# Kernel tuning notes

Measured on AMD Instinct MI355X. Metric: run time of the kernel, lower is better.

## Reference

```python
import jax, jax.numpy as jnp
import numpy as np

N = 100000   # nodes
E = 600000   # edges
DIN = 128
H = 128
DOUT = 64
EPS = 1e-5   # BatchNorm1d default eps


def setup_inputs() -> dict:
    key = jax.random.key(0)
    ks = jax.random.split(key, 16)
    w = lambda k, shape: jax.random.normal(k, shape, jnp.float32) * 0.05
    return {
        "x": jax.random.normal(ks[0], (N, DIN), jnp.float32),
        "edge_index": jax.random.randint(ks[1], (2, E), 0, N),
        # layer 1: SAGEConv(DIN -> H)  (lin_l on aggregated neighbors w/ bias, lin_r on root)
        "Wl1": w(ks[2], (DIN, H)), "bl1": jnp.zeros((H,), jnp.float32), "Wr1": w(ks[3], (DIN, H)),
        "g1": jnp.ones((H,), jnp.float32), "be1": jnp.zeros((H,), jnp.float32),
        "rm1": jax.random.normal(ks[4], (H,), jnp.float32) * 0.1,
        "rv1": jax.random.uniform(ks[5], (H,), jnp.float32, 0.5, 1.5),
        # layer 2: SAGEConv(H -> H)
        "Wl2": w(ks[6], (H, H)), "bl2": jnp.zeros((H,), jnp.float32), "Wr2": w(ks[7], (H, H)),
        "g2": jnp.ones((H,), jnp.float32), "be2": jnp.zeros((H,), jnp.float32),
        "rm2": jax.random.normal(ks[8], (H,), jnp.float32) * 0.1,
        "rv2": jax.random.uniform(ks[9], (H,), jnp.float32, 0.5, 1.5),
        # layer 3: SAGEConv(H -> DOUT), no BN/ReLU after
        "Wl3": w(ks[10], (H, DOUT)), "bl3": jnp.zeros((DOUT,), jnp.float32), "Wr3": w(ks[11], (H, DOUT)),
    }


def _sage_conv(x, src, dst, Wl, bl, Wr):
    # mean-aggregate source features at targets, then lin_l(agg) + b + lin_r(x)
    agg = jax.ops.segment_sum(x[src], dst, num_segments=N)          # [N, d]
    deg = jax.ops.segment_sum(jnp.ones((src.shape[0],), x.dtype), dst, num_segments=N)
    agg = agg / jnp.maximum(deg, 1.0)[:, None]
    return agg @ Wl + bl + x @ Wr


def _bn_eval(h, g, b, rm, rv):
    return (h - rm) * (g * jax.lax.rsqrt(rv + EPS)) + b


def reference(x, edge_index, Wl1, bl1, Wr1, g1, be1, rm1, rv1,
              Wl2, bl2, Wr2, g2, be2, rm2, rv2, Wl3, bl3, Wr3):
    src, dst = edge_index[0], edge_index[1]
    h = jax.nn.relu(_bn_eval(_sage_conv(x, src, dst, Wl1, bl1, Wr1), g1, be1, rm1, rv1))
    h = jax.nn.relu(_bn_eval(_sage_conv(h, src, dst, Wl2, bl2, Wr2), g2, be2, rm2, rv2))
    return _sage_conv(h, src, dst, Wl3, bl3, Wr3)   # [N, DOUT]
```

## Files before the change

### kernel.cpp

```cpp
#include <hip/hip_runtime.h>

#define CAP 48

typedef short  s8v  __attribute__((ext_vector_type(8)));
typedef float  f4v  __attribute__((ext_vector_type(4)));

__device__ __forceinline__ unsigned short f2bf(float f) {
    unsigned u = __float_as_uint(f);
    u += 0x7FFFu + ((u >> 16) & 1u);
    return (unsigned short)(u >> 16);
}
__device__ __forceinline__ float bflo(unsigned v) { return __uint_as_float(v << 16); }
__device__ __forceinline__ float bfhi(unsigned v) { return __uint_as_float(v & 0xffff0000u); }

__global__ __launch_bounds__(256) void k_bucket(const int* __restrict__ src, const int* __restrict__ dst,
                                                int E, int* __restrict__ cnt, int* __restrict__ bucket) {
    int e = blockIdx.x * 256 + threadIdx.x;
    if (e < E) {
        int d = dst[e];
        int slot = atomicAdd(&cnt[d], 1);
        if (slot < CAP) bucket[(size_t)d * CAP + slot] = src[e];
    }
}

__global__ void k_prep(const float* g1, const float* be1, const float* rm1, const float* rv1, const float* bl1,
                       const float* g2, const float* be2, const float* rm2, const float* rv2, const float* bl2,
                       float* P) {
    int j = threadIdx.x;
    float s1 = g1[j] * rsqrtf(rv1[j] + 1e-5f);
    P[j]       = s1;
    P[128 + j] = (bl1[j] - rm1[j]) * s1 + be1[j];
    float s2 = g2[j] * rsqrtf(rv2[j] + 1e-5f);
    P[256 + j] = s2;
    P[384 + j] = (bl2[j] - rm2[j]) * s2 + be2[j];
}

__global__ __launch_bounds__(256) void k_cvt(const float* __restrict__ in, unsigned short* __restrict__ out, int n4) {
    int i = blockIdx.x * 256 + threadIdx.x;
    if (i < n4) {
        float4 v = ((const float4*)in)[i];
        ushort4 o;
        o.x = f2bf(v.x); o.y = f2bf(v.y); o.z = f2bf(v.z); o.w = f2bf(v.w);
        ((ushort4*)out)[i] = o;
    }
}

__global__ __launch_bounds__(256) void k_packW(const float* W0, const float* W1, const float* W2,
                                               const float* W3, const float* W4, const float* W5,
                                               unsigned short* P0, unsigned short* P1, unsigned short* P2,
                                               unsigned short* P3, unsigned short* P4, unsigned short* P5) {
    const float* W; unsigned short* P; int JD;
    switch (blockIdx.y) {
        case 0: W = W0; P = P0; JD = 128; break;
        case 1: W = W1; P = P1; JD = 128; break;
        case 2: W = W2; P = P2; JD = 128; break;
        case 3: W = W3; P = P3; JD = 128; break;
        case 4: W = W4; P = P4; JD = 64;  break;
        default:W = W5; P = P5; JD = 64;  break;
    }
    int o = blockIdx.x * 256 + threadIdx.x;
    if (o >= 128 * JD) return;
    int j    = o & 7;
    int lane = (o >> 3) & 63;
    int t    = o >> 9;
    int nt   = t % (JD / 16);
    int kt   = t / (JD / 16);
    int k = kt * 32 + (lane >> 4) * 8 + j;
    int n = nt * 16 + (lane & 15);
    P[o] = f2bf(W[(size_t)k * JD + n]);
}

__global__ __launch_bounds__(256) void k_agg128b(const unsigned short* __restrict__ in, const int* __restrict__ cnt,
                                                 const int* __restrict__ bucket, uint2* __restrict__ out, int n) {
    int wv   = (blockIdx.x * 256 + threadIdx.x) >> 6;
    int lane = threadIdx.x & 63;
    int g    = lane >> 5;
    int li   = lane & 31;
    int node = wv * 2 + g;
    if (node >= n) return;
    int c = cnt[node]; if (c > CAP) c = CAP;
    const uint2* inp = (const uint2*)in;
    int idxv = 0;
    if (li < c) idxv = bucket[(size_t)node * CAP + li];
    float a0 = 0.f, a1 = 0.f, a2 = 0.f, a3 = 0.f;
    const int base = g << 5;
    int cc = c < 32 ? c : 32;
    int s = 0;
    for (; s + 4 <= cc; s += 4) {
        int i0 = __shfl(idxv, base + s);
        int i1 = __shfl(idxv, base + s + 1);
        int i2 = __shfl(idxv, base + s + 2);
        int i3 = __shfl(idxv, base + s + 3);
        uint2 v0 = inp[(size_t)i0 * 32 + li];
        uint2 v1 = inp[(size_t)i1 * 32 + li];
        uint2 v2 = inp[(size_t)i2 * 32 + li];
        uint2 v3 = inp[(size_t)i3 * 32 + li];
        a0 += bflo(v0.x) + bflo(v1.x) + bflo(v2.x) + bflo(v3.x);
        a1 += bfhi(v0.x) + bfhi(v1.x) + bfhi(v2.x) + bfhi(v3.x);
        a2 += bflo(v0.y) + bflo(v1.y) + bflo(v2.y) + bflo(v3.y);
        a3 += bfhi(v0.y) + bfhi(v1.y) + bfhi(v2.y) + bfhi(v3.y);
    }
    for (; s < cc; s++) {
        int i0 = __shfl(idxv, base + s);
        uint2 v0 = inp[(size_t)i0 * 32 + li];
        a0 += bflo(v0.x); a1 += bfhi(v0.x); a2 += bflo(v0.y); a3 += bfhi(v0.y);
    }
    for (; s < c; s++) {
        int i0 = bucket[(size_t)node * CAP + s];
        uint2 v0 = inp[(size_t)i0 * 32 + li];
        a0 += bflo(v0.x); a1 += bfhi(v0.x); a2 += bflo(v0.y); a3 += bfhi(v0.y);
    }
    float iv = 1.0f / fmaxf((float)c, 1.0f);
    a0 *= iv; a1 *= iv; a2 *= iv; a3 *= iv;
    uint2 o;
    o.x = (unsigned)f2bf(a0) | ((unsigned)f2bf(a1) << 16);
    o.y = (unsigned)f2bf(a2) | ((unsigned)f2bf(a3) << 16);
    out[(size_t)node * 32 + li] = o;
}

__global__ __launch_bounds__(256) void k_agg64b(const unsigned short* __restrict__ in, const int* __restrict__ cnt,
                                                const int* __restrict__ bucket, float4* __restrict__ out, int n) {
    int wv   = (blockIdx.x * 256 + threadIdx.x) >> 6;
    int lane = threadIdx.x & 63;
    int g    = lane >> 4;
    int li   = lane & 15;
    int node = wv * 4 + g;
    if (node >= n) return;
    int c = cnt[node]; if (c > CAP) c = CAP;
    const uint2* inp = (const uint2*)in;
    int idxv = 0;
    if (li < c) idxv = bucket[(size_t)node * CAP + li];
    float a0 = 0.f, a1 = 0.f, a2 = 0.f, a3 = 0.f;
    const int base = g << 4;
    int cc = c < 16 ? c : 16;
    int s = 0;
    for (; s + 4 <= cc; s += 4) {
        int i0 = __shfl(idxv, base + s);
        int i1 = __shfl(idxv, base + s + 1);
        int i2 = __shfl(idxv, base + s + 2);
        int i3 = __shfl(idxv, base + s + 3);
        uint2 v0 = inp[(size_t)i0 * 16 + li];
        uint2 v1 = inp[(size_t)i1 * 16 + li];
        uint2 v2 = inp[(size_t)i2 * 16 + li];
        uint2 v3 = inp[(size_t)i3 * 16 + li];
        a0 += bflo(v0.x) + bflo(v1.x) + bflo(v2.x) + bflo(v3.x);
        a1 += bfhi(v0.x) + bfhi(v1.x) + bfhi(v2.x) + bfhi(v3.x);
        a2 += bflo(v0.y) + bflo(v1.y) + bflo(v2.y) + bflo(v3.y);
        a3 += bfhi(v0.y) + bfhi(v1.y) + bfhi(v2.y) + bfhi(v3.y);
    }
    for (; s < cc; s++) {
        int i0 = __shfl(idxv, base + s);
        uint2 v0 = inp[(size_t)i0 * 16 + li];
        a0 += bflo(v0.x); a1 += bfhi(v0.x); a2 += bflo(v0.y); a3 += bfhi(v0.y);
    }
    for (; s < c; s++) {
        int i0 = bucket[(size_t)node * CAP + s];
        uint2 v0 = inp[(size_t)i0 * 16 + li];
        a0 += bflo(v0.x); a1 += bfhi(v0.x); a2 += bflo(v0.y); a3 += bfhi(v0.y);
    }
    float iv = 1.0f / fmaxf((float)c, 1.0f);
    float4 o; o.x = a0 * iv; o.y = a1 * iv; o.z = a2 * iv; o.w = a3 * iv;
    out[(size_t)node * 16 + li] = o;
}

template<int JD, bool DUAL, bool RELU, bool ADDD, bool BIAS, bool OUTF, bool OUTB>
__global__ __launch_bounds__(256) void k_mfma(const unsigned short* __restrict__ A, const unsigned short* __restrict__ Bp,
                                              const unsigned short* __restrict__ A2, const unsigned short* __restrict__ B2p,
                                              const float* __restrict__ Dadd, const float* __restrict__ scale,
                                              const float* __restrict__ shift, float* __restrict__ outf,
                                              unsigned short* __restrict__ outb, int nrows) {
    constexpr int NT = JD / 16;
    constexpr int CW = JD / 32;
    constexpr int RG = 4 / CW;
    const int tid  = threadIdx.x;
    const int wave = tid >> 6;
    const int lane = tid & 63;
    const int cgrp = wave % CW;
    const int rgrp = wave / CW;
    const int rw0  = (blockIdx.x * RG + rgrp) * 32;
    if (rw0 >= nrows) return;

    const int m = lane & 15;
    const int q = lane >> 4;
    const int rA0 = min(rw0 + m,      nrows - 1);
    const int rA1 = min(rw0 + 16 + m, nrows - 1);
    const int nt0 = cgrp * 2;

    f4v acc[2][2];
    #pragma unroll
    for (int mt = 0; mt < 2; mt++)
        #pragma unroll
        for (int c = 0; c < 2; c++) {
            acc[mt][c][0] = 0.f; acc[mt][c][1] = 0.f; acc[mt][c][2] = 0.f; acc[mt][c][3] = 0.f;
        }

    #pragma unroll
    for (int kt = 0; kt < 4; kt++) {
        const int ko = kt * 32 + q * 8;
        s8v a0 = *(const s8v*)(A + (size_t)rA0 * 128 + ko);
        s8v a1 = *(const s8v*)(A + (size_t)rA1 * 128 + ko);
        #pragma unroll
        for (int c = 0; c < 2; c++) {
            s8v b = *(const s8v*)(Bp + ((size_t)(kt * NT + nt0 + c) * 64 + lane) * 8);
            acc[0][c] = __builtin_amdgcn_mfma_f32_16x16x32_bf16(a0, b, acc[0][c], 0, 0, 0);
            acc[1][c] = __builtin_amdgcn_mfma_f32_16x16x32_bf16(a1, b, acc[1][c], 0, 0, 0);
        }
        if constexpr (DUAL) {
            s8v a0d = *(const s8v*)(A2 + (size_t)rA0 * 128 + ko);
            s8v a1d = *(const s8v*)(A2 + (size_t)rA1 * 128 + ko);
            #pragma unroll
            for (int c = 0; c < 2; c++) {
                s8v b2 = *(const s8v*)(B2p + ((size_t)(kt * NT + nt0 + c) * 64 + lane) * 8);
                acc[0][c] = __builtin_amdgcn_mfma_f32_16x16x32_bf16(a0d, b2, acc[0][c], 0, 0, 0);
                acc[1][c] = __builtin_amdgcn_mfma_f32_16x16x32_bf16(a1d, b2, acc[1][c], 0, 0, 0);
            }
        }
    }

    float scv[2], shv[2];
    #pragma unroll
    for (int c = 0; c < 2; c++) {
        int col = (nt0 + c) * 16 + m;
        if constexpr (RELU) scv[c] = scale[col];
        if constexpr (RELU || BIAS) shv[c] = shift[col];
    }
    #pragma unroll
    for (int mt = 0; mt < 2; mt++) {
        #pragma unroll
        for (int reg = 0; reg < 4; reg++) {
            int row = rw0 + mt * 16 + q * 4 + reg;
            if (row < nrows) {
                #pragma unroll
                for (int c = 0; c < 2; c++) {
                    int col = (nt0 + c) * 16 + m;
                    float v = acc[mt][c][reg];
                    if constexpr (ADDD) v += Dadd[(size_t)row * JD + col];
                    if constexpr (BIAS) v += shv[c];
                    if constexpr (RELU) v = fmaxf(v * scv[c] + shv[c], 0.f);
                    if constexpr (OUTF) outf[(size_t)row * JD + col] = v;
                    if constexpr (OUTB) outb[(size_t)row * JD + col] = f2bf(v);
                }
            }
        }
    }
}

extern "C" void kernel_launch(void* const* d_in, const int* in_sizes, int n_in,
                              void* d_out, int out_size, void* d_ws, size_t ws_size,
                              hipStream_t stream) {
    const float* x   = (const float*)d_in[0];
    const int*   ei  = (const int*)d_in[1];
    const float* Wl1 = (const float*)d_in[2];
    const float* bl1 = (const float*)d_in[3];
    const float* Wr1 = (const float*)d_in[4];
    const float* g1  = (const float*)d_in[5];
    const float* be1 = (const float*)d_in[6];
    const float* rm1 = (const float*)d_in[7];
    const float* rv1 = (const float*)d_in[8];
    const float* Wl2 = (const float*)d_in[9];
    const float* bl2 = (const float*)d_in[10];
    const float* Wr2 = (const float*)d_in[11];
    const float* g2  = (const float*)d_in[12];
    const float* be2 = (const float*)d_in[13];
    const float* rm2 = (const float*)d_in[14];
    const float* rv2 = (const float*)d_in[15];
    const float* Wl3 = (const float*)d_in[16];
    const float* bl3 = (const float*)d_in[17];
    const float* Wr3 = (const float*)d_in[18];

    const int N = in_sizes[0] / 128;
    const int E = in_sizes[1] / 2;
    const int* src = ei;
    const int* dst = ei + E;

    char* w = (char*)d_ws;
    auto au = [](size_t v) { return (v + 1023) & ~(size_t)1023; };
    size_t off = 0;
    int*            cnt    = (int*)(w + off);            off += au((size_t)N * 4);
    int*            bucket = (int*)(w + off);            off += au((size_t)N * CAP * 4);
    unsigned short* xb     = (unsigned short*)(w + off); off += au((size_t)N * 128 * 2);
    unsigned short* aggb   = (unsigned short*)(w + off); off += au((size_t)N * 128 * 2);
    unsigned short* hb     = (unsigned short*)(w + off); off += au((size_t)N * 128 * 2);
    unsigned short* hb2    = (unsigned short*)(w + off); off += au((size_t)N * 128 * 2);
    unsigned short* t3b    = (unsigned short*)(w + off); off += au((size_t)N * 64 * 2);
    float*          agg3   = (float*)(w + off);          off += au((size_t)N * 64 * 4);
    unsigned short* Wp[6];
    Wp[0] = (unsigned short*)(w + off); off += au(128 * 128 * 2);
    Wp[1] = (unsigned short*)(w + off); off += au(128 * 128 * 2);
    Wp[2] = (unsigned short*)(w + off); off += au(128 * 128 * 2);
    Wp[3] = (unsigned short*)(w + off); off += au(128 * 128 * 2);
    Wp[4] = (unsigned short*)(w + off); off += au(128 * 64 * 2);
    Wp[5] = (unsigned short*)(w + off); off += au(128 * 64 * 2);
    float* P = (float*)(w + off); off += 2048;
    (void)ws_size; (void)n_in;

    hipMemsetAsync(cnt, 0, (size_t)N * 4, stream);
    k_bucket<<<(E + 255) / 256, 256, 0, stream>>>(src, dst, E, cnt, bucket);
    k_prep<<<1, 128, 0, stream>>>(g1, be1, rm1, rv1, bl1, g2, be2, rm2, rv2, bl2, P);
    dim3 pg(64, 6);
    k_packW<<<pg, 256, 0, stream>>>(Wl1, Wr1, Wl2, Wr2, Wl3, Wr3,
                                    Wp[0], Wp[1], Wp[2], Wp[3], Wp[4], Wp[5]);
    k_cvt<<<((N * 128 / 4) + 255) / 256, 256, 0, stream>>>(x, xb, N * 128 / 4);

    const int agg128Grid = ((size_t)N * 32 + 255) / 256;
    const int agg64Grid  = ((size_t)N * 16 + 255) / 256;
    const int gemmGrid128 = (N + 31) / 32;
    const int gemmGrid64  = (N + 63) / 64;

    k_agg128b<<<agg128Grid, 256, 0, stream>>>(xb, cnt, bucket, (uint2*)aggb, N);
    k_mfma<128, true, true, false, false, false, true><<<gemmGrid128, 256, 0, stream>>>(
        aggb, Wp[0], xb, Wp[1], nullptr, P, P + 128, nullptr, hb, N);

    k_agg128b<<<agg128Grid, 256, 0, stream>>>(hb, cnt, bucket, (uint2*)aggb, N);
    k_mfma<128, true, true, false, false, false, true><<<gemmGrid128, 256, 0, stream>>>(
        aggb, Wp[2], hb, Wp[3], nullptr, P + 256, P + 384, nullptr, hb2, N);

    k_mfma<64, false, false, false, false, false, true><<<gemmGrid64, 256, 0, stream>>>(
        hb2, Wp[4], nullptr, nullptr, nullptr, nullptr, nullptr, nullptr, t3b, N);
    k_agg64b<<<agg64Grid, 256, 0, stream>>>(t3b, cnt, bucket, (float4*)agg3, N);
    k_mfma<64, false, false, true, true, true, false><<<gemmGrid64, 256, 0, stream>>>(
        hb2, Wp[5], nullptr, nullptr, agg3, nullptr, bl3, (float*)d_out, nullptr, N);
}
```

Before: 346.8 us.

## Fuse neighbor aggregation into MFMA GEMM kernels via shared-memory tiles

```diff
diff --git a/kernel.cpp b/kernel.cpp
--- a/kernel.cpp
+++ b/kernel.cpp
@@ -23,40 +23,33 @@
     }
 }
 
-__global__ void k_prep(const float* g1, const float* be1, const float* rm1, const float* rv1, const float* bl1,
-                       const float* g2, const float* be2, const float* rm2, const float* rv2, const float* bl2,
-                       float* P) {
-    int j = threadIdx.x;
-    float s1 = g1[j] * rsqrtf(rv1[j] + 1e-5f);
-    P[j]       = s1;
-    P[128 + j] = (bl1[j] - rm1[j]) * s1 + be1[j];
-    float s2 = g2[j] * rsqrtf(rv2[j] + 1e-5f);
-    P[256 + j] = s2;
-    P[384 + j] = (bl2[j] - rm2[j]) * s2 + be2[j];
-}
-
-__global__ __launch_bounds__(256) void k_cvt(const float* __restrict__ in, unsigned short* __restrict__ out, int n4) {
-    int i = blockIdx.x * 256 + threadIdx.x;
-    if (i < n4) {
-        float4 v = ((const float4*)in)[i];
-        ushort4 o;
-        o.x = f2bf(v.x); o.y = f2bf(v.y); o.z = f2bf(v.z); o.w = f2bf(v.w);
-        ((ushort4*)out)[i] = o;
-    }
-}
-
-__global__ __launch_bounds__(256) void k_packW(const float* W0, const float* W1, const float* W2,
-                                               const float* W3, const float* W4, const float* W5,
-                                               unsigned short* P0, unsigned short* P1, unsigned short* P2,
-                                               unsigned short* P3, unsigned short* P4, unsigned short* P5) {
-    const float* W; unsigned short* P; int JD;
+__global__ __launch_bounds__(256) void k_prepack(const float* W0, const float* W1, const float* W2,
+                                                 const float* W3, const float* W4, const float* W5,
+                                                 unsigned short* P0, unsigned short* P1, unsigned short* P2,
+                                                 unsigned short* P3, unsigned short* P4, unsigned short* P5,
+                                                 const float* g1, const float* be1, const float* rm1, const float* rv1, const float* bl1,
+                                                 const float* g2, const float* be2, const float* rm2, const float* rv2, const float* bl2,
+                                                 float* P) {
+    if (blockIdx.y == 6) {
+        if (blockIdx.x == 0 && threadIdx.x < 128) {
+            int j = threadIdx.x;
+            float s1 = g1[j] * rsqrtf(rv1[j] + 1e-5f);
+            P[j]       = s1;
+            P[128 + j] = (bl1[j] - rm1[j]) * s1 + be1[j];
+            float s2 = g2[j] * rsqrtf(rv2[j] + 1e-5f);
+            P[256 + j] = s2;
+            P[384 + j] = (bl2[j] - rm2[j]) * s2 + be2[j];
+        }
+        return;
+    }
+    const float* W; unsigned short* Pk; int JD;
     switch (blockIdx.y) {
-        case 0: W = W0; P = P0; JD = 128; break;
-        case 1: W = W1; P = P1; JD = 128; break;
-        case 2: W = W2; P = P2; JD = 128; break;
-        case 3: W = W3; P = P3; JD = 128; break;
-        case 4: W = W4; P = P4; JD = 64;  break;
-        default:W = W5; P = P5; JD = 64;  break;
+        case 0: W = W0; Pk = P0; JD = 128; break;
+        case 1: W = W1; Pk = P1; JD = 128; break;
+        case 2: W = W2; Pk = P2; JD = 128; break;
+        case 3: W = W3; Pk = P3; JD = 128; break;
+        case 4: W = W4; Pk = P4; JD = 64;  break;
+        default:W = W5; Pk = P5; JD = 64;  break;
     }
     int o = blockIdx.x * 256 + threadIdx.x;
     if (o >= 128 * JD) return;
@@ -67,124 +60,90 @@
     int kt   = t / (JD / 16);
     int k = kt * 32 + (lane >> 4) * 8 + j;
     int n = nt * 16 + (lane & 15);
-    P[o] = f2bf(W[(size_t)k * JD + n]);
-}
-
-__global__ __launch_bounds__(256) void k_agg128b(const unsigned short* __restrict__ in, const int* __restrict__ cnt,
-                                                 const int* __restrict__ bucket, uint2* __restrict__ out, int n) {
-    int wv   = (blockIdx.x * 256 + threadIdx.x) >> 6;
-    int lane = threadIdx.x & 63;
-    int g    = lane >> 5;
-    int li   = lane & 31;
-    int node = wv * 2 + g;
-    if (node >= n) return;
-    int c = cnt[node]; if (c > CAP) c = CAP;
-    const uint2* inp = (const uint2*)in;
-    int idxv = 0;
-    if (li < c) idxv = bucket[(size_t)node * CAP + li];
-    float a0 = 0.f, a1 = 0.f, a2 = 0.f, a3 = 0.f;
-    const int base = g << 5;
-    int cc = c < 32 ? c : 32;
-    int s = 0;
-    for (; s + 4 <= cc; s += 4) {
-        int i0 = __shfl(idxv, base + s);
-        int i1 = __shfl(idxv, base + s + 1);
-        int i2 = __shfl(idxv, base + s + 2);
-        int i3 = __shfl(idxv, base + s + 3);
-        uint2 v0 = inp[(size_t)i0 * 32 + li];
-        uint2 v1 = inp[(size_t)i1 * 32 + li];
-        uint2 v2 = inp[(size_t)i2 * 32 + li];
-        uint2 v3 = inp[(size_t)i3 * 32 + li];
-        a0 += bflo(v0.x) + bflo(v1.x) + bflo(v2.x) + bflo(v3.x);
-        a1 += bfhi(v0.x) + bfhi(v1.x) + bfhi(v2.x) + bfhi(v3.x);
-        a2 += bflo(v0.y) + bflo(v1.y) + bflo(v2.y) + bflo(v3.y);
-        a3 += bfhi(v0.y) + bfhi(v1.y) + bfhi(v2.y) + bfhi(v3.y);
-    }
-    for (; s < cc; s++) {
-        int i0 = __shfl(idxv, base + s);
-        uint2 v0 = inp[(size_t)i0 * 32 + li];
-        a0 += bflo(v0.x); a1 += bfhi(v0.x); a2 += bflo(v0.y); a3 += bfhi(v0.y);
-    }
-    for (; s < c; s++) {
-        int i0 = bucket[(size_t)node * CAP + s];
-        uint2 v0 = inp[(size_t)i0 * 32 + li];
-        a0 += bflo(v0.x); a1 += bfhi(v0.x); a2 += bflo(v0.y); a3 += bfhi(v0.y);
-    }
-    float iv = 1.0f / fmaxf((float)c, 1.0f);
-    a0 *= iv; a1 *= iv; a2 *= iv; a3 *= iv;
-    uint2 o;
-    o.x = (unsigned)f2bf(a0) | ((unsigned)f2bf(a1) << 16);
-    o.y = (unsigned)f2bf(a2) | ((unsigned)f2bf(a3) << 16);
-    out[(size_t)node * 32 + li] = o;
-}
-
-__global__ __launch_bounds__(256) void k_agg64b(const unsigned short* __restrict__ in, const int* __restrict__ cnt,
-                                                const int* __restrict__ bucket, float4* __restrict__ out, int n) {
-    int wv   = (blockIdx.x * 256 + threadIdx.x) >> 6;
-    int lane = threadIdx.x & 63;
-    int g    = lane >> 4;
-    int li   = lane & 15;
-    int node = wv * 4 + g;
-    if (node >= n) return;
-    int c = cnt[node]; if (c > CAP) c = CAP;
-    const uint2* inp = (const uint2*)in;
-    int idxv = 0;
-    if (li < c) idxv = bucket[(size_t)node * CAP + li];
-    float a0 = 0.f, a1 = 0.f, a2 = 0.f, a3 = 0.f;
-    const int base = g << 4;
-    int cc = c < 16 ? c : 16;
-    int s = 0;
-    for (; s + 4 <= cc; s += 4) {
-        int i0 = __shfl(idxv, base + s);
-        int i1 = __shfl(idxv, base + s + 1);
-        int i2 = __shfl(idxv, base + s + 2);
-        int i3 = __shfl(idxv, base + s + 3);
-        uint2 v0 = inp[(size_t)i0 * 16 + li];
-        uint2 v1 = inp[(size_t)i1 * 16 + li];
-        uint2 v2 = inp[(size_t)i2 * 16 + li];
-        uint2 v3 = inp[(size_t)i3 * 16 + li];
-        a0 += bflo(v0.x) + bflo(v1.x) + bflo(v2.x) + bflo(v3.x);
-        a1 += bfhi(v0.x) + bfhi(v1.x) + bfhi(v2.x) + bfhi(v3.x);
-        a2 += bflo(v0.y) + bflo(v1.y) + bflo(v2.y) + bflo(v3.y);
-        a3 += bfhi(v0.y) + bfhi(v1.y) + bfhi(v2.y) + bfhi(v3.y);
-    }
-    for (; s < cc; s++) {
-        int i0 = __shfl(idxv, base + s);
-        uint2 v0 = inp[(size_t)i0 * 16 + li];
-        a0 += bflo(v0.x); a1 += bfhi(v0.x); a2 += bflo(v0.y); a3 += bfhi(v0.y);
-    }
-    for (; s < c; s++) {
-        int i0 = bucket[(size_t)node * CAP + s];
-        uint2 v0 = inp[(size_t)i0 * 16 + li];
-        a0 += bflo(v0.x); a1 += bfhi(v0.x); a2 += bflo(v0.y); a3 += bfhi(v0.y);
-    }
-    float iv = 1.0f / fmaxf((float)c, 1.0f);
-    float4 o; o.x = a0 * iv; o.y = a1 * iv; o.z = a2 * iv; o.w = a3 * iv;
-    out[(size_t)node * 16 + li] = o;
-}
-
-template<int JD, bool DUAL, bool RELU, bool ADDD, bool BIAS, bool OUTF, bool OUTB>
-__global__ __launch_bounds__(256) void k_mfma(const unsigned short* __restrict__ A, const unsigned short* __restrict__ Bp,
-                                              const unsigned short* __restrict__ A2, const unsigned short* __restrict__ B2p,
-                                              const float* __restrict__ Dadd, const float* __restrict__ scale,
-                                              const float* __restrict__ shift, float* __restrict__ outf,
-                                              unsigned short* __restrict__ outb, int nrows) {
-    constexpr int NT = JD / 16;
-    constexpr int CW = JD / 32;
-    constexpr int RG = 4 / CW;
+    Pk[o] = f2bf(W[(size_t)k * JD + n]);
+}
+
+__global__ __launch_bounds__(256) void k_cvt(const float* __restrict__ in, unsigned short* __restrict__ out, int n4) {
+    int i = blockIdx.x * 256 + threadIdx.x;
+    if (i < n4) {
+        float4 v = ((const float4*)in)[i];
+        ushort4 o;
+        o.x = f2bf(v.x); o.y = f2bf(v.y); o.z = f2bf(v.z); o.w = f2bf(v.w);
+        ((ushort4*)out)[i] = o;
+    }
+}
+
+template<bool T3>
+__global__ __launch_bounds__(256) void k_fused(const unsigned short* __restrict__ feat,
+                                               const int* __restrict__ cnt, const int* __restrict__ bucket,
+                                               const unsigned short* __restrict__ Bl, const unsigned short* __restrict__ Br,
+                                               const float* __restrict__ scale, const float* __restrict__ shift,
+                                               unsigned short* __restrict__ out,
+                                               const unsigned short* __restrict__ W3p, unsigned short* __restrict__ t3,
+                                               int n) {
+    __shared__ unsigned short sA[32 * 136];
+    __shared__ unsigned short sH[T3 ? 32 * 136 : 8];
     const int tid  = threadIdx.x;
     const int wave = tid >> 6;
     const int lane = tid & 63;
-    const int cgrp = wave % CW;
-    const int rgrp = wave / CW;
-    const int rw0  = (blockIdx.x * RG + rgrp) * 32;
-    if (rw0 >= nrows) return;
+    const int nb0  = blockIdx.x * 32;
+    if (nb0 >= n) return;
+
+    {
+        const int g  = lane >> 5;
+        const int li = lane & 31;
+        const uint2* inp = (const uint2*)feat;
+        const int base = g << 5;
+        #pragma unroll
+        for (int p = 0; p < 4; p++) {
+            int row  = wave * 8 + p * 2 + g;
+            int node = nb0 + row;
+            if (node < n) {
+                int c = cnt[node]; if (c > CAP) c = CAP;
+                int idxv = 0;
+                if (li < c) idxv = bucket[(size_t)node * CAP + li];
+                float a0 = 0.f, a1 = 0.f, a2 = 0.f, a3 = 0.f;
+                int cc = c < 32 ? c : 32;
+                int s = 0;
+                for (; s + 4 <= cc; s += 4) {
+                    int i0 = __shfl(idxv, base + s);
+                    int i1 = __shfl(idxv, base + s + 1);
+                    int i2 = __shfl(idxv, base + s + 2);
+                    int i3 = __shfl(idxv, base + s + 3);
+                    uint2 v0 = inp[(size_t)i0 * 32 + li];
+                    uint2 v1 = inp[(size_t)i1 * 32 + li];
+                    uint2 v2 = inp[(size_t)i2 * 32 + li];
+                    uint2 v3 = inp[(size_t)i3 * 32 + li];
+                    a0 += bflo(v0.x) + bflo(v1.x) + bflo(v2.x) + bflo(v3.x);
+                    a1 += bfhi(v0.x) + bfhi(v1.x) + bfhi(v2.x) + bfhi(v3.x);
+                    a2 += bflo(v0.y) + bflo(v1.y) + bflo(v2.y) + bflo(v3.y);
+                    a3 += bfhi(v0.y) + bfhi(v1.y) + bfhi(v2.y) + bfhi(v3.y);
+                }
+                for (; s < cc; s++) {
+                    int i0 = __shfl(idxv, base + s);
+                    uint2 v0 = inp[(size_t)i0 * 32 + li];
+                    a0 += bflo(v0.x); a1 += bfhi(v0.x); a2 += bflo(v0.y); a3 += bfhi(v0.y);
+                }
+                for (; s < c; s++) {
+                    int i0 = bucket[(size_t)node * CAP + s];
+                    uint2 v0 = inp[(size_t)i0 * 32 + li];
+                    a0 += bflo(v0.x); a1 += bfhi(v0.x); a2 += bflo(v0.y); a3 += bfhi(v0.y);
+                }
+                float iv = 1.0f / fmaxf((float)c, 1.0f);
+                uint2 o;
+                o.x = (unsigned)f2bf(a0 * iv) | ((unsigned)f2bf(a1 * iv) << 16);
+                o.y = (unsigned)f2bf(a2 * iv) | ((unsigned)f2bf(a3 * iv) << 16);
+                ((uint2*)(sA + row * 136))[li] = o;
+            }
+        }
+    }
+    __syncthreads();
 
     const int m = lane & 15;
     const int q = lane >> 4;
-    const int rA0 = min(rw0 + m,      nrows - 1);
-    const int rA1 = min(rw0 + 16 + m, nrows - 1);
-    const int nt0 = cgrp * 2;
+    const int nt0 = wave * 2;
+    const int rg0 = min(nb0 + m,      n - 1);
+    const int rg1 = min(nb0 + 16 + m, n - 1);
 
     f4v acc[2][2];
     #pragma unroll
@@ -197,23 +156,18 @@
     #pragma unroll
     for (int kt = 0; kt < 4; kt++) {
         const int ko = kt * 32 + q * 8;
-        s8v a0 = *(const s8v*)(A + (size_t)rA0 * 128 + ko);
-        s8v a1 = *(const s8v*)(A + (size_t)rA1 * 128 + ko);
+        s8v a0 = *(const s8v*)(sA + m * 136 + ko);
+        s8v a1 = *(const s8v*)(sA + (16 + m) * 136 + ko);
+        s8v a0d = *(const s8v*)(feat + (size_t)rg0 * 128 + ko);
+        s8v a1d = *(const s8v*)(feat + (size_t)rg1 * 128 + ko);
         #pragma unroll
         for (int c = 0; c < 2; c++) {
-            s8v b = *(const s8v*)(Bp + ((size_t)(kt * NT + nt0 + c) * 64 + lane) * 8);
+            s8v b  = *(const s8v*)(Bl + ((size_t)(kt * 8 + nt0 + c) * 64 + lane) * 8);
             acc[0][c] = __builtin_amdgcn_mfma_f32_16x16x32_bf16(a0, b, acc[0][c], 0, 0, 0);
             acc[1][c] = __builtin_amdgcn_mfma_f32_16x16x32_bf16(a1, b, acc[1][c], 0, 0, 0);
-        }
-        if constexpr (DUAL) {
-            s8v a0d = *(const s8v*)(A2 + (size_t)rA0 * 128 + ko);
-            s8v a1d = *(const s8v*)(A2 + (size_t)rA1 * 128 + ko);
-            #pragma unroll
-            for (int c = 0; c < 2; c++) {
-                s8v b2 = *(const s8v*)(B2p + ((size_t)(kt * NT + nt0 + c) * 64 + lane) * 8);
-                acc[0][c] = __builtin_amdgcn_mfma_f32_16x16x32_bf16(a0d, b2, acc[0][c], 0, 0, 0);
-                acc[1][c] = __builtin_amdgcn_mfma_f32_16x16x32_bf16(a1d, b2, acc[1][c], 0, 0, 0);
-            }
+            s8v b2 = *(const s8v*)(Br + ((size_t)(kt * 8 + nt0 + c) * 64 + lane) * 8);
+            acc[0][c] = __builtin_amdgcn_mfma_f32_16x16x32_bf16(a0d, b2, acc[0][c], 0, 0, 0);
+            acc[1][c] = __builtin_amdgcn_mfma_f32_16x16x32_bf16(a1d, b2, acc[1][c], 0, 0, 0);
         }
     }
 
@@ -221,26 +175,140 @@
     #pragma unroll
     for (int c = 0; c < 2; c++) {
         int col = (nt0 + c) * 16 + m;
-        if constexpr (RELU) scv[c] = scale[col];
-        if constexpr (RELU || BIAS) shv[c] = shift[col];
+        scv[c] = scale[col]; shv[c] = shift[col];
     }
     #pragma unroll
     for (int mt = 0; mt < 2; mt++) {
         #pragma unroll
         for (int reg = 0; reg < 4; reg++) {
-            int row = rw0 + mt * 16 + q * 4 + reg;
-            if (row < nrows) {
+            int rloc = mt * 16 + q * 4 + reg;
+            int row  = nb0 + rloc;
+            if (row < n) {
                 #pragma unroll
                 for (int c = 0; c < 2; c++) {
                     int col = (nt0 + c) * 16 + m;
-                    float v = acc[mt][c][reg];
-                    if constexpr (ADDD) v += Dadd[(size_t)row * JD + col];
-                    if constexpr (BIAS) v += shv[c];
-                    if constexpr (RELU) v = fmaxf(v * scv[c] + shv[c], 0.f);
-                    if constexpr (OUTF) outf[(size_t)row * JD + col] = v;
-                    if constexpr (OUTB) outb[(size_t)row * JD + col] = f2bf(v);
+                    float v = fmaxf(acc[mt][c][reg] * scv[c] + shv[c], 0.f);
+                    unsigned short u = f2bf(v);
+                    out[(size_t)row * 128 + col] = u;
+                    if constexpr (T3) sH[rloc * 136 + col] = u;
                 }
             }
+        }
+    }
+
+    if constexpr (T3) {
+        __syncthreads();
+        f4v a3c[2];
+        #pragma unroll
+        for (int mt = 0; mt < 2; mt++) { a3c[mt][0] = 0.f; a3c[mt][1] = 0.f; a3c[mt][2] = 0.f; a3c[mt][3] = 0.f; }
+        #pragma unroll
+        for (int kt = 0; kt < 4; kt++) {
+            const int ko = kt * 32 + q * 8;
+            s8v a0 = *(const s8v*)(sH + m * 136 + ko);
+            s8v a1 = *(const s8v*)(sH + (16 + m) * 136 + ko);
+            s8v b  = *(const s8v*)(W3p + ((size_t)(kt * 4 + wave) * 64 + lane) * 8);
+            a3c[0] = __builtin_amdgcn_mfma_f32_16x16x32_bf16(a0, b, a3c[0], 0, 0, 0);
+            a3c[1] = __builtin_amdgcn_mfma_f32_16x16x32_bf16(a1, b, a3c[1], 0, 0, 0);
+        }
+        #pragma unroll
+        for (int mt = 0; mt < 2; mt++) {
+            #pragma unroll
+            for (int reg = 0; reg < 4; reg++) {
+                int row = nb0 + mt * 16 + q * 4 + reg;
+                if (row < n) t3[(size_t)row * 64 + wave * 16 + m] = f2bf(a3c[mt][reg]);
+            }
+        }
+    }
+}
+
+__global__ __launch_bounds__(256) void k_final(const unsigned short* __restrict__ hb2,
+                                               const unsigned short* __restrict__ t3,
+                                               const int* __restrict__ cnt, const int* __restrict__ bucket,
+                                               const unsigned short* __restrict__ Bp, const float* __restrict__ bias,
+                                               float* __restrict__ outf, int n) {
+    __shared__ float sG[32 * 68];
+    const int tid  = threadIdx.x;
+    const int wave = tid >> 6;
+    const int lane = tid & 63;
+    const int nb0  = blockIdx.x * 32;
+    if (nb0 >= n) return;
+
+    {
+        const int g  = lane >> 4;
+        const int li = lane & 15;
+        const uint2* inp = (const uint2*)t3;
+        const int base = g << 4;
+        #pragma unroll
+        for (int p = 0; p < 2; p++) {
+            int row  = wave * 8 + p * 4 + g;
+            int node = nb0 + row;
+            if (node < n) {
+                int c = cnt[node]; if (c > CAP) c = CAP;
+                int idxv = 0;
+                if (li < c) idxv = bucket[(size_t)node * CAP + li];
+                float a0 = 0.f, a1 = 0.f, a2 = 0.f, a3 = 0.f;
+                int cc = c < 16 ? c : 16;
+                int s = 0;
+                for (; s + 4 <= cc; s += 4) {
+                    int i0 = __shfl(idxv, base + s);
+                    int i1 = __shfl(idxv, base + s + 1);
+                    int i2 = __shfl(idxv, base + s + 2);
+                    int i3 = __shfl(idxv, base + s + 3);
+                    uint2 v0 = inp[(size_t)i0 * 16 + li];
+                    uint2 v1 = inp[(size_t)i1 * 16 + li];
+                    uint2 v2 = inp[(size_t)i2 * 16 + li];
+                    uint2 v3 = inp[(size_t)i3 * 16 + li];
+                    a0 += bflo(v0.x) + bflo(v1.x) + bflo(v2.x) + bflo(v3.x);
+                    a1 += bfhi(v0.x) + bfhi(v1.x) + bfhi(v2.x) + bfhi(v3.x);
+                    a2 += bflo(v0.y) + bflo(v1.y) + bflo(v2.y) + bflo(v3.y);
+                    a3 += bfhi(v0.y) + bfhi(v1.y) + bfhi(v2.y) + bfhi(v3.y);
+                }
+                for (; s < cc; s++) {
+                    int i0 = __shfl(idxv, base + s);
+                    uint2 v0 = inp[(size_t)i0 * 16 + li];
+                    a0 += bflo(v0.x); a1 += bfhi(v0.x); a2 += bflo(v0.y); a3 += bfhi(v0.y);
+                }
+                for (; s < c; s++) {
+                    int i0 = bucket[(size_t)node * CAP + s];
+                    uint2 v0 = inp[(size_t)i0 * 16 + li];
+                    a0 += bflo(v0.x); a1 += bfhi(v0.x); a2 += bflo(v0.y); a3 += bfhi(v0.y);
+                }
+                float iv = 1.0f / fmaxf((float)c, 1.0f);
+                float4 o; o.x = a0 * iv; o.y = a1 * iv; o.z = a2 * iv; o.w = a3 * iv;
+                ((float4*)(sG + row * 68))[li] = o;
+            }
+        }
+    }
+    __syncthreads();
+
+    const int m = lane & 15;
+    const int q = lane >> 4;
+    const int rg0 = min(nb0 + m,      n - 1);
+    const int rg1 = min(nb0 + 16 + m, n - 1);
+
+    f4v acc[2];
+    #pragma unroll
+    for (int mt = 0; mt < 2; mt++) { acc[mt][0] = 0.f; acc[mt][1] = 0.f; acc[mt][2] = 0.f; acc[mt][3] = 0.f; }
+
+    #pragma unroll
+    for (int kt = 0; kt < 4; kt++) {
+        const int ko = kt * 32 + q * 8;
+        s8v a0 = *(const s8v*)(hb2 + (size_t)rg0 * 128 + ko);
+        s8v a1 = *(const s8v*)(hb2 + (size_t)rg1 * 128 + ko);
+        s8v b  = *(const s8v*)(Bp + ((size_t)(kt * 4 + wave) * 64 + lane) * 8);
+        acc[0] = __builtin_amdgcn_mfma_f32_16x16x32_bf16(a0, b, acc[0], 0, 0, 0);
+        acc[1] = __builtin_amdgcn_mfma_f32_16x16x32_bf16(a1, b, acc[1], 0, 0, 0);
+    }
+
+    const int col = wave * 16 + m;
+    const float bv = bias[col];
+    #pragma unroll
+    for (int mt = 0; mt < 2; mt++) {
+        #pragma unroll
+        for (int reg = 0; reg < 4; reg++) {
+            int rloc = mt * 16 + q * 4 + reg;
+            int row  = nb0 + rloc;
+            if (row < n) outf[(size_t)row * 64 + col] = acc[mt][reg] + sG[rloc * 68 + col] + bv;
         }
     }
 }
@@ -279,11 +347,9 @@
     int*            cnt    = (int*)(w + off);            off += au((size_t)N * 4);
     int*            bucket = (int*)(w + off);            off += au((size_t)N * CAP * 4);
     unsigned short* xb     = (unsigned short*)(w + off); off += au((size_t)N * 128 * 2);
-    unsigned short* aggb   = (unsigned short*)(w + off); off += au((size_t)N * 128 * 2);
     unsigned short* hb     = (unsigned short*)(w + off); off += au((size_t)N * 128 * 2);
     unsigned short* hb2    = (unsigned short*)(w + off); off += au((size_t)N * 128 * 2);
     unsigned short* t3b    = (unsigned short*)(w + off); off += au((size_t)N * 64 * 2);
-    float*          agg3   = (float*)(w + off);          off += au((size_t)N * 64 * 4);
     unsigned short* Wp[6];
     Wp[0] = (unsigned short*)(w + off); off += au(128 * 128 * 2);
     Wp[1] = (unsigned short*)(w + off); off += au(128 * 128 * 2);
@@ -296,28 +362,17 @@
 
     hipMemsetAsync(cnt, 0, (size_t)N * 4, stream);
     k_bucket<<<(E + 255) / 256, 256, 0, stream>>>(src, dst, E, cnt, bucket);
-    k_prep<<<1, 128, 0, stream>>>(g1, be1, rm1, rv1, bl1, g2, be2, rm2, rv2, bl2, P);
-    dim3 pg(64, 6);
-    k_packW<<<pg, 256, 0, stream>>>(Wl1, Wr1, Wl2, Wr2, Wl3, Wr3,
-                                    Wp[0], Wp[1], Wp[2], Wp[3], Wp[4], Wp[5]);
+    dim3 pg(64, 7);
+    k_prepack<<<pg, 256, 0, stream>>>(Wl1, Wr1, Wl2, Wr2, Wl3, Wr3,
+                                      Wp[0], Wp[1], Wp[2], Wp[3], Wp[4], Wp[5],
+                                      g1, be1, rm1, rv1, bl1, g2, be2, rm2, rv2, bl2, P);
     k_cvt<<<((N * 128 / 4) + 255) / 256, 256, 0, stream>>>(x, xb, N * 128 / 4);
 
-    const int agg128Grid = ((size_t)N * 32 + 255) / 256;
-    const int agg64Grid  = ((size_t)N * 16 + 255) / 256;
-    const int gemmGrid128 = (N + 31) / 32;
-    const int gemmGrid64  = (N + 63) / 64;
-
-    k_agg128b<<<agg128Grid, 256, 0, stream>>>(xb, cnt, bucket, (uint2*)aggb, N);
-    k_mfma<128, true, true, false, false, false, true><<<gemmGrid128, 256, 0, stream>>>(
-        aggb, Wp[0], xb, Wp[1], nullptr, P, P + 128, nullptr, hb, N);
-
-    k_agg128b<<<agg128Grid, 256, 0, stream>>>(hb, cnt, bucket, (uint2*)aggb, N);
-    k_mfma<128, true, true, false, false, false, true><<<gemmGrid128, 256, 0, stream>>>(
-        aggb, Wp[2], hb, Wp[3], nullptr, P + 256, P + 384, nullptr, hb2, N);
-
-    k_mfma<64, false, false, false, false, false, true><<<gemmGrid64, 256, 0, stream>>>(
-        hb2, Wp[4], nullptr, nullptr, nullptr, nullptr, nullptr, nullptr, t3b, N);
-    k_agg64b<<<agg64Grid, 256, 0, stream>>>(t3b, cnt, bucket, (float4*)agg3, N);
-    k_mfma<64, false, false, true, true, true, false><<<gemmGrid64, 256, 0, stream>>>(
-        hb2, Wp[5], nullptr, nullptr, agg3, nullptr, bl3, (float*)d_out, nullptr, N);
-}
+    const int grid = (N + 31) / 32;
+
+    k_fused<false><<<grid, 256, 0, stream>>>(xb, cnt, bucket, Wp[0], Wp[1],
+                                             P, P + 128, hb, nullptr, nullptr, N);
+    k_fused<true><<<grid, 256, 0, stream>>>(hb, cnt, bucket, Wp[2], Wp[3],
+                                            P + 256, P + 384, hb2, Wp[4], t3b, N);
+    k_final<<<grid, 256, 0, stream>>>(hb2, t3b, cnt, bucket, Wp[5], bl3, (float*)d_out, N);
+}
```

After: 296.3 us. 14.6% less time.
